# Performance work log

Hardware: AMD Instinct MI355X
Metric: run time of the kernel (lower is better)

## Reference

```python
import jax, jax.numpy as jnp
import numpy as np

B, C, H, W = 16, 16, 96, 320


def _hat(phi):
    z = jnp.zeros_like(phi[..., 0])
    px, py, pz = phi[..., 0], phi[..., 1], phi[..., 2]
    return jnp.stack([
        jnp.stack([z, -pz, py], -1),
        jnp.stack([pz, z, -px], -1),
        jnp.stack([-py, px, z], -1)], -2)


def se3_exp(xi):
    # xi: [B,6] twist (rho, phi) -> [B,4,4] SE3 matrix
    rho, phi = xi[:, :3], xi[:, 3:6]
    th2 = jnp.sum(phi * phi, -1)
    small = th2 < 1e-8
    th2s = jnp.where(small, 1.0, th2)
    th = jnp.sqrt(th2s)
    A = jnp.where(small, 1.0 - th2 / 6.0, jnp.sin(th) / th)
    Bc = jnp.where(small, 0.5 - th2 / 24.0, (1.0 - jnp.cos(th)) / th2s)
    Cc = jnp.where(small, 1.0 / 6.0 - th2 / 120.0, (th - jnp.sin(th)) / (th2s * th))
    K = _hat(phi)
    K2 = K @ K
    I = jnp.eye(3, dtype=xi.dtype)
    R = I + A[:, None, None] * K + Bc[:, None, None] * K2
    V = I + Bc[:, None, None] * K + Cc[:, None, None] * K2
    t = V @ rho[..., None]
    top = jnp.concatenate([R, t], -1)
    bot = jnp.broadcast_to(jnp.array([0.0, 0.0, 0.0, 1.0], xi.dtype), (xi.shape[0], 1, 4))
    return jnp.concatenate([top, bot], 1)


def grid_sample(im, grid):
    # torch F.grid_sample: bilinear, padding_mode='zeros', align_corners=False
    Bb, Cc, Hh, Ww = im.shape
    x = (grid[..., 0] + 1.0) * (Ww * 0.5) - 0.5
    y = (grid[..., 1] + 1.0) * (Hh * 0.5) - 0.5
    x0 = jnp.floor(x); y0 = jnp.floor(y)
    wx = x - x0; wy = y - y0
    x0i = x0.astype(jnp.int32); y0i = y0.astype(jnp.int32)

    def one(imb, x0b, y0b, wxb, wyb):
        def g(ix, iy):
            valid = ((ix >= 0) & (ix < Ww) & (iy >= 0) & (iy < Hh)).astype(imb.dtype)
            v = imb[:, jnp.clip(iy, 0, Hh - 1), jnp.clip(ix, 0, Ww - 1)]
            return v * valid[None]
        v00 = g(x0b, y0b); v01 = g(x0b + 1, y0b)
        v10 = g(x0b, y0b + 1); v11 = g(x0b + 1, y0b + 1)
        wxb = wxb[None]; wyb = wyb[None]
        return (v00 * (1 - wxb) * (1 - wyb) + v01 * wxb * (1 - wyb)
                + v10 * (1 - wxb) * wyb + v11 * wxb * wyb)

    return jax.vmap(one)(im, x0i, y0i, wx, wy)


def setup_inputs():
    key = jax.random.key(0)
    ks = jax.random.split(key, 10)
    # projected pixel coords (center) + 4 finite-difference taps
    xc = jax.random.uniform(ks[0], (B, H, W), jnp.float32, 2.0, W - 3.0)
    yc = jax.random.uniform(ks[1], (B, H, W), jnp.float32, 2.0, H - 3.0)
    xs = jnp.stack([xc, xc + 1, xc - 1, xc, xc], 1)
    ys = jnp.stack([yc, yc, yc, yc + 1, yc - 1], 1)
    p2 = jnp.stack([xs, ys], 1)[:, :, None]  # [B,2,1,5,H,W]
    XY = jax.random.normal(ks[2], (B, 2, H * W)) * 2.0
    Z = 1.0 + 10.0 * jax.random.uniform(ks[3], (B, 1, H * W))
    P2 = jnp.concatenate([XY, Z], 1)  # [B,3,HW], Z > 0
    f = 250.0 + 50.0 * jax.random.uniform(ks[4], (B,))
    K = jnp.zeros((B, 3, 3)).at[:, 0, 0].set(f).at[:, 1, 1].set(f)
    K = K.at[:, 0, 2].set(W / 2).at[:, 1, 2].set(H / 2).at[:, 2, 2].set(1.0)
    poses = se3_exp(0.1 * jax.random.normal(ks[5], (B, 6)))
    return dict(
        poses=poses, calib_K=K, p2=p2, P2=P2,
        weight=jax.random.uniform(ks[6], (B, 1, H, W), jnp.float32, 0.2, 1.0),
        src_feat=jax.random.normal(ks[7], (B, C, H, W)),
        tgt_feat=jax.random.normal(ks[8], (B, C, H, W)),
        src_w=jax.random.uniform(ks[9], (B, 1, H, W), jnp.float32, 0.3, 1.0),
        tgt_w=jax.random.uniform(jax.random.fold_in(key, 11), (B, 1, H, W), jnp.float32, 0.3, 1.0),
    )


def reference(poses, calib_K, p2, P2, weight, src_feat, tgt_feat, src_w, tgt_w):
    Bb, Cc, Hh, Ww = src_feat.shape
    HW = Hh * Ww
    # --- sample_tgt ---
    grid_pix = p2.transpose(2, 0, 4, 5, 3, 1).reshape(Bb, HW, 5, 2)  # n1 == 1
    gx = 2 * (grid_pix[..., :1] + 0.5) / Ww - 1
    gy = 2 * (grid_pix[..., 1:] + 0.5) / Hh - 1
    grid = jnp.concatenate([gx, gy], -1)  # [B,HW,5,2]
    f = grid_sample(tgt_feat, grid).reshape(Bb, Cc, Hh, Ww, 5)
    warped_tgt_feat = f[..., 0]
    grads = jnp.stack([(f[..., 1] - f[..., 2]) * 0.5,
                       (f[..., 3] - f[..., 4]) * 0.5], -1)  # [B,C,H,W,2]
    warped_tgt_w = grid_sample(tgt_w, grid[:, :, :1]).reshape(Bb, 1, Hh, Ww)
    # --- per-pixel 2x6 pixel->pose Jacobian ---
    X, Y, Z = P2[:, 0], P2[:, 1], P2[:, 2]  # [B,HW]
    fx = calib_K[:, 0, 0][:, None]; fy = calib_K[:, 1, 1][:, None]
    fxZ = fx / Z; fyZ = fy / Z
    fxXZ2 = fxZ * X / Z; fyYZ2 = fyZ * Y / Z
    zeros = jnp.zeros_like(fxXZ2)
    row0 = jnp.stack([fxZ, zeros, -fxXZ2, -fxXZ2 * Y, fx + fxXZ2 * X, -fxZ * Y], 1)
    row1 = jnp.stack([zeros, fyZ, -fyYZ2, -fy - fyYZ2 * Y, fyYZ2 * X, fyZ * X], 1)
    J_pixel_xi = jnp.stack([row0, row1], 1).transpose(0, 3, 1, 2)  # [B,HW,2,6]
    J_img_pixel = grads.reshape(Bb, Cc, HW, 2).transpose(0, 2, 1, 3)  # [B,HW,C,2]
    J = -(J_img_pixel @ J_pixel_xi)  # [B,HW,C,6]
    res = (src_feat - warped_tgt_feat).transpose(0, 2, 3, 1).reshape(Bb, HW, Cc)
    w = (src_w * warped_tgt_w * weight).reshape(Bb, HW)
    JW = J * w[:, :, None, None]
    Hm = jnp.einsum('bpck,bpcl->bkl', JW, J)  # [B,6,6] Gauss-Newton Hessian
    b = -jnp.einsum('bpc,bpck->bk', res, JW)  # [B,6]
    # H is SPD (sum of w*J^T J, w>0): solve == cholesky_solve of the original
    update = jnp.linalg.solve(Hm, b[..., None])[..., 0]  # [B,6]
    new_poses = se3_exp(update) @ poses
    return new_poses, update
```

## Files before the change

### kernel.cpp

```cpp
#include <hip/hip_runtime.h>
#include <math.h>

#if __has_builtin(__builtin_amdgcn_cvt_scalef32_pk_f32_fp4) && __has_builtin(__builtin_amdgcn_cvt_scalef32_pk_fp4_f32)
#define HAVE_FP4 1
#else
#define HAVE_FP4 0
#endif

#define BATCH 16
#define CHN   16
#define IMH   96
#define IMW   320
#define HW    (IMH*IMW)
#define NBLK  (HW/256)
#define NPART 27
#define TWB   (HW*4)
#if HAVE_FP4
#define RECB  (HW*16)
#else
#define MAPB  (HW*16)
#endif

typedef __attribute__((ext_vector_type(2))) float f32x2;

__device__ __forceinline__ int comp4(int4 v, int k) {
    switch (k) { case 0: return v.x; case 1: return v.y; case 2: return v.z; default: return v.w; }
}

__device__ __forceinline__ float dpp_row_sum(float x) {
    union fi { float f; int i; };
    fi v; v.f = x;
#define DPPSTEP(CTRL) { fi t; t.i = __builtin_amdgcn_update_dpp(0, v.i, CTRL, 0xf, 0xf, true); v.f += t.f; }
    DPPSTEP(0x111)
    DPPSTEP(0x112)
    DPPSTEP(0x114)
    DPPSTEP(0x118)
#undef DPPSTEP
    return v.f;
}

__global__ __launch_bounds__(256) void build_maps(const float* __restrict__ in,
                                                  const float* __restrict__ tw,
                                                  char* __restrict__ dst,
                                                  char* __restrict__ twr) {
    const int b = blockIdx.y;
    const int p = blockIdx.x * 256 + threadIdx.x;
    const int y = p / IMW, x = p - y * IMW;
    const float* ip = in + (size_t)b * CHN * HW + p;
    float f[16];
#pragma unroll
    for (int c = 0; c < 16; ++c) f[c] = ip[c * HW];

#if HAVE_FP4
    unsigned d0 = 0, d1 = 0;
    d0 = __builtin_amdgcn_cvt_scalef32_pk_fp4_f32(d0, f[0],  f[1],  1.0f, 0);
    d0 = __builtin_amdgcn_cvt_scalef32_pk_fp4_f32(d0, f[2],  f[3],  1.0f, 1);
    d0 = __builtin_amdgcn_cvt_scalef32_pk_fp4_f32(d0, f[4],  f[5],  1.0f, 2);
    d0 = __builtin_amdgcn_cvt_scalef32_pk_fp4_f32(d0, f[6],  f[7],  1.0f, 3);
    d1 = __builtin_amdgcn_cvt_scalef32_pk_fp4_f32(d1, f[8],  f[9],  1.0f, 0);
    d1 = __builtin_amdgcn_cvt_scalef32_pk_fp4_f32(d1, f[10], f[11], 1.0f, 1);
    d1 = __builtin_amdgcn_cvt_scalef32_pk_fp4_f32(d1, f[12], f[13], 1.0f, 2);
    d1 = __builtin_amdgcn_cvt_scalef32_pk_fp4_f32(d1, f[14], f[15], 1.0f, 3);
    int2 lv; lv.x = (int)d0; lv.y = (int)d1;
    char* rb = dst + (size_t)b * RECB;
    *(int2*)(rb + (size_t)p * 16) = lv;
    if (y > 0)        *(int2*)(rb + (size_t)(p - IMW) * 16 + 8) = lv;
    if (y == IMH - 1) *(int2*)(rb + (size_t)p * 16 + 8) = lv;
#else
    int4 pk;
    int* pw = &pk.x;
#pragma unroll
    for (int k = 0; k < 4; ++k) {
        int dw = __builtin_amdgcn_cvt_pk_fp8_f32(f[4 * k + 0], f[4 * k + 1], 0, false);
        dw     = __builtin_amdgcn_cvt_pk_fp8_f32(f[4 * k + 2], f[4 * k + 3], dw, true);
        pw[k] = dw;
    }
    *(int4*)(dst + (size_t)b * MAPB + ((size_t)(y >> 1) * IMW + x) * 32 + (y & 1) * 16) = pk;
#endif

    const float* twb = tw + (size_t)b * HW;
    const int xp1 = min(x + 1, IMW - 1), yp1 = min(y + 1, IMH - 1);
    const float v00 = twb[p];
    const float v01 = twb[y * IMW + xp1];
    const float v10 = twb[yp1 * IMW + x];
    const float v11 = twb[yp1 * IMW + xp1];
    int wq = __builtin_amdgcn_cvt_pk_fp8_f32(v00, v01, 0, false);
    wq     = __builtin_amdgcn_cvt_pk_fp8_f32(v10, v11, wq, true);
    ((int*)(twr + (size_t)b * TWB))[p] = wq;
}

__global__ __launch_bounds__(256, 2) void gn_accum(
    const float* __restrict__ p2,
    const float* __restrict__ P2,
    const float* __restrict__ calibK,
    const float* __restrict__ weight,
    const float* __restrict__ src_feat,
    const float* __restrict__ src_w,
    const char* __restrict__ twr,
    const char* __restrict__ fmap,
    float* __restrict__ partials)
{
    __shared__ float xs_l[1280];
    __shared__ float ys_l[1280];
    __shared__ float red[16][NPART];

    const int n   = blockIdx.x;
    const int b   = n & 15;
    const int blk = n >> 4;
    const int t   = threadIdx.x;
    const int p   = blk * 256 + t;

    const unsigned Gblk0 = ((unsigned)b * HW + (unsigned)(blk * 256)) * 5u;
#pragma unroll
    for (int j = 0; j < 5; ++j) {
        const unsigned idx  = (unsigned)(j * 256 + t);
        const unsigned G    = Gblk0 + idx;
        const unsigned sBig = G / (unsigned)(BATCH * HW);
        const unsigned r    = G - sBig * (unsigned)(BATCH * HW);
        const unsigned bb   = r / (unsigned)HW;
        const unsigned q    = r - bb * (unsigned)HW;
        const float* pb = p2 + (size_t)bb * (10 * HW) + (size_t)sBig * HW + q;
        xs_l[idx] = pb[0];
        ys_l[idx] = pb[5 * HW];
    }
    __syncthreads();

    float wxs[5], wys[5];
    int   twoff = 0;
#if HAVE_FP4
    int off[5];
#else
    int offA[5], offC[5];
#endif
#pragma unroll
    for (int s = 0; s < 5; ++s) {
        const float xp = xs_l[5 * t + s];
        const float yp = ys_l[5 * t + s];
        float gx = 2.0f * (xp + 0.5f) / (float)IMW - 1.0f;
        float gy = 2.0f * (yp + 0.5f) / (float)IMH - 1.0f;
        float x  = (gx + 1.0f) * ((float)IMW * 0.5f) - 0.5f;
        float y  = (gy + 1.0f) * ((float)IMH * 0.5f) - 0.5f;
        float x0 = floorf(x), y0 = floorf(y);
        wxs[s] = x - x0;
        wys[s] = y - y0;
        int xi = (int)x0, yi = (int)y0;
        xi = min(max(xi, 0), IMW - 2);
        yi = min(max(yi, 0), IMH - 2);
#if HAVE_FP4
        off[s] = (yi * IMW + xi) * 16;
#else
        const int h0 = yi >> 1, par0 = yi & 1;
        const int h1 = h0 + par0, par1 = par0 ^ 1;
        offA[s] = (h0 * IMW + xi) * 32 + par0 * 16;
        offC[s] = (h1 * IMW + xi) * 32 + par1 * 16;
#endif
        if (s == 0) twoff = (yi * IMW + xi) * 4;
    }

#if HAVE_FP4
    const char* mapb = fmap + (size_t)b * RECB;
    int4 L0[5], L1[5];
#pragma unroll
    for (int s = 0; s < 5; ++s) {
        L0[s] = *(const int4*)(mapb + off[s]);
        L1[s] = *(const int4*)(mapb + off[s] + 16);
    }
#else
    const char* mapb = fmap + (size_t)b * MAPB;
    int4 LA[5], LB[5], LC[5], LD[5];
#pragma unroll
    for (int s = 0; s < 5; ++s) {
        LA[s] = *(const int4*)(mapb + offA[s]);
        LB[s] = *(const int4*)(mapb + offA[s] + 32);
        LC[s] = *(const int4*)(mapb + offC[s]);
        LD[s] = *(const int4*)(mapb + offC[s] + 32);
    }
#endif
    const int twq = *(const int*)(twr + (size_t)b * TWB + twoff);

    float srcv[16];
    const float* srcb = src_feat + (size_t)b * CHN * HW + p;
#pragma unroll
    for (int c = 0; c < 16; ++c) srcv[c] = srcb[c * HW];

    const float* P2b = P2 + (size_t)b * 3 * HW;
    const float X = P2b[p], Y = P2b[HW + p], Z = P2b[2 * HW + p];
    const float wP  = weight[(size_t)b * HW + p];
    const float swP = src_w[(size_t)b * HW + p];

    const float fx = calibK[b * 9 + 0];
    const float fy = calibK[b * 9 + 4];
    const float fxZ = fx / Z, fyZ = fy / Z;
    const float fxXZ2 = fxZ * X / Z;
    const float fyYZ2 = fyZ * Y / Z;
    float r0[6] = { fxZ, 0.0f, -fxXZ2, -fxXZ2 * Y, fx + fxXZ2 * X, -fxZ * Y };
    float r1[6] = { 0.0f, fyZ, -fyYZ2, -fy - fyYZ2 * Y, fyYZ2 * X, fyZ * X };

    float w00[5], w01[5], w10[5], w11[5];
#pragma unroll
    for (int s = 0; s < 5; ++s) {
        float wx = wxs[s], wy = wys[s];
        w00[s] = (1.0f - wx) * (1.0f - wy);
        w01[s] = wx * (1.0f - wy);
        w10[s] = (1.0f - wx) * wy;
        w11[s] = wx * wy;
    }

    float wtw;
    {
        const float wx = wxs[0], wy = wys[0];
        f32x2 wlo = __builtin_amdgcn_cvt_pk_f32_fp8(twq, false);
        f32x2 whi = __builtin_amdgcn_cvt_pk_f32_fp8(twq, true);
        wtw = wlo[0] * (1.0f - wx) * (1.0f - wy) + wlo[1] * wx * (1.0f - wy)
            + whi[0] * (1.0f - wx) * wy          + whi[1] * wx * wy;
    }
    const float w = swP * wtw * wP;

    f32x2 SxxV = {0.f,0.f}, SxyV = {0.f,0.f}, SyyV = {0.f,0.f}, TxV = {0.f,0.f}, TyV = {0.f,0.f};
#if HAVE_FP4
#define PAIRSTEP(H, K) {                                                          \
        f32x2 fsv[5];                                                             \
        _Pragma("unroll")                                                         \
        for (int s = 0; s < 5; ++s) {                                             \
            const int ad = (H) ? L0[s].y : L0[s].x;                               \
            const int bd = (H) ? L1[s].y : L1[s].x;                               \
            const int cd = (H) ? L0[s].w : L0[s].z;                               \
            const int dd = (H) ? L1[s].w : L1[s].z;                               \
            fsv[s] = __builtin_amdgcn_cvt_scalef32_pk_f32_fp4(ad, 1.0f, K) * w00[s] \
                   + __builtin_amdgcn_cvt_scalef32_pk_f32_fp4(bd, 1.0f, K) * w01[s] \
                   + __builtin_amdgcn_cvt_scalef32_pk_f32_fp4(cd, 1.0f, K) * w10[s] \
                   + __builtin_amdgcn_cvt_scalef32_pk_f32_fp4(dd, 1.0f, K) * w11[s]; \
        }                                                                         \
        const f32x2 sr = { srcv[(H) * 8 + 2 * (K)], srcv[(H) * 8 + 2 * (K) + 1] };\
        f32x2 resv = sr - fsv[0];                                                 \
        f32x2 gxv  = (fsv[1] - fsv[2]) * 0.5f;                                    \
        f32x2 gyv  = (fsv[3] - fsv[4]) * 0.5f;                                    \
        SxxV += gxv * gxv; SxyV += gxv * gyv; SyyV += gyv * gyv;                  \
        TxV  += resv * gxv; TyV += resv * gyv; }
    PAIRSTEP(0, 0) PAIRSTEP(0, 1) PAIRSTEP(0, 2) PAIRSTEP(0, 3)
    PAIRSTEP(1, 0) PAIRSTEP(1, 1) PAIRSTEP(1, 2) PAIRSTEP(1, 3)
#undef PAIRSTEP
#else
#pragma unroll
    for (int k = 0; k < 4; ++k) {
        f32x2 flo[5], fhi[5];
#pragma unroll
        for (int s = 0; s < 5; ++s) {
            const int a = comp4(LA[s], k), bq = comp4(LB[s], k);
            const int c = comp4(LC[s], k), d  = comp4(LD[s], k);
            flo[s] = __builtin_amdgcn_cvt_pk_f32_fp8(a,  false) * w00[s]
                   + __builtin_amdgcn_cvt_pk_f32_fp8(bq, false) * w01[s]
                   + __builtin_amdgcn_cvt_pk_f32_fp8(c,  false) * w10[s]
                   + __builtin_amdgcn_cvt_pk_f32_fp8(d,  false) * w11[s];
            fhi[s] = __builtin_amdgcn_cvt_pk_f32_fp8(a,  true)  * w00[s]
                   + __builtin_amdgcn_cvt_pk_f32_fp8(bq, true)  * w01[s]
                   + __builtin_amdgcn_cvt_pk_f32_fp8(c,  true)  * w10[s]
                   + __builtin_amdgcn_cvt_pk_f32_fp8(d,  true)  * w11[s];
        }
        const f32x2 srcl = { srcv[4 * k + 0], srcv[4 * k + 1] };
        const f32x2 srch = { srcv[4 * k + 2], srcv[4 * k + 3] };
        f32x2 resl = srcl - flo[0];
        f32x2 gxl  = (flo[1] - flo[2]) * 0.5f;
        f32x2 gyl  = (flo[3] - flo[4]) * 0.5f;
        SxxV += gxl * gxl; SxyV += gxl * gyl; SyyV += gyl * gyl;
        TxV  += resl * gxl; TyV += resl * gyl;
        f32x2 resh = srch - fhi[0];
        f32x2 gxh  = (fhi[1] - fhi[2]) * 0.5f;
        f32x2 gyh  = (fhi[3] - fhi[4]) * 0.5f;
        SxxV += gxh * gxh; SxyV += gxh * gyh; SyyV += gyh * gyh;
        TxV  += resh * gxh; TyV += resh * gyh;
    }
#endif
    const float Sxx = SxxV[0] + SxxV[1];
    const float Sxy = SxyV[0] + SxyV[1];
    const float Syy = SyyV[0] + SyyV[1];
    const float Tx  = TxV[0]  + TxV[1];
    const float Ty  = TyV[0]  + TyV[1];

    const float Pm = w * Sxx, Qm = w * Sxy, Rm = w * Syy;
    const float tx = w * Tx,  ty = w * Ty;

    float av[6], cv[6];
#pragma unroll
    for (int k = 0; k < 6; ++k) {
        av[k] = Pm * r0[k] + Qm * r1[k];
        cv[k] = Qm * r0[k] + Rm * r1[k];
    }

    const int wv   = t >> 6;
    const int lane = t & 63;
    const int rrow = (wv << 2) | (lane >> 4);
    const bool wr  = (lane & 15) == 15;

    int idx = 0;
#pragma unroll
    for (int k = 0; k < 6; ++k) {
#pragma unroll
        for (int l = 0; l < 6; ++l) {
            if (l < k) continue;
            float v = r0[k] * av[l] + r1[k] * cv[l];
            v = dpp_row_sum(v);
            if (wr) red[rrow][idx] = v;
            ++idx;
        }
    }
#pragma unroll
    for (int k = 0; k < 6; ++k) {
        float v = tx * r0[k] + ty * r1[k];
        v = dpp_row_sum(v);
        if (wr) red[rrow][21 + k] = v;
    }
    __syncthreads();
    if (t < NPART) {
        float s = 0.0f;
#pragma unroll
        for (int r = 0; r < 16; ++r) s += red[r][t];
        partials[((size_t)b * NBLK + blk) * NPART + t] = s;
    }
}

__global__ __launch_bounds__(256) void gn_solve(
    const float* __restrict__ partials,
    const float* __restrict__ poses,
    float* __restrict__ out)
{
    const int b = blockIdx.x;
    const int t = threadIdx.x;
    __shared__ double dsum[8][NPART];
    __shared__ double sums[NPART];

    if (t < 216) {
        const int col = t % NPART;
        const int g   = t / NPART;
        double s = 0.0;
        for (int j = g; j < NBLK; j += 8)
            s += (double)partials[((size_t)b * NBLK + j) * NPART + col];
        dsum[g][col] = s;
    }
    __syncthreads();
    if (t < NPART) {
        double s = 0.0;
#pragma unroll
        for (int g = 0; g < 8; ++g) s += dsum[g][t];
        sums[t] = s;
    }
    __syncthreads();
    if (t != 0) return;

    double A[6][7];
    {
        int idx = 0;
        for (int k = 0; k < 6; ++k)
            for (int l = k; l < 6; ++l) {
                A[k][l] = sums[idx];
                A[l][k] = sums[idx];
                ++idx;
            }
        for (int k = 0; k < 6; ++k) A[k][6] = sums[21 + k];
    }
    for (int col = 0; col < 6; ++col) {
        int piv = col; double mx = fabs(A[col][col]);
        for (int rr = col + 1; rr < 6; ++rr) {
            double v = fabs(A[rr][col]);
            if (v > mx) { mx = v; piv = rr; }
        }
        if (piv != col)
            for (int j = col; j < 7; ++j) { double tmp = A[col][j]; A[col][j] = A[piv][j]; A[piv][j] = tmp; }
        double d = A[col][col];
        for (int rr = col + 1; rr < 6; ++rr) {
            double f = A[rr][col] / d;
            for (int j = col; j < 7; ++j) A[rr][j] -= f * A[col][j];
        }
    }
    double x[6];
    for (int i = 5; i >= 0; --i) {
        double s = A[i][6];
        for (int j = i + 1; j < 6; ++j) s -= A[i][j] * x[j];
        x[i] = s / A[i][i];
    }

    const double rho[3] = { x[0], x[1], x[2] };
    const double phi[3] = { x[3], x[4], x[5] };
    const double th2 = phi[0]*phi[0] + phi[1]*phi[1] + phi[2]*phi[2];
    const bool small = th2 < 1e-8;
    const double th2s = small ? 1.0 : th2;
    const double th = sqrt(th2s);
    const double Ac = small ? 1.0 - th2 / 6.0   : sin(th) / th;
    const double Bc = small ? 0.5 - th2 / 24.0  : (1.0 - cos(th)) / th2s;
    const double Cc = small ? 1.0/6.0 - th2/120.0 : (th - sin(th)) / (th2s * th);
    const double Kh[3][3] = { { 0.0, -phi[2],  phi[1] },
                              {  phi[2], 0.0, -phi[0] },
                              { -phi[1],  phi[0], 0.0 } };
    double K2[3][3];
    for (int i = 0; i < 3; ++i)
        for (int j = 0; j < 3; ++j) {
            double s = 0.0;
            for (int k = 0; k < 3; ++k) s += Kh[i][k] * Kh[k][j];
            K2[i][j] = s;
        }
    double T[4][4];
    for (int i = 0; i < 3; ++i)
        for (int j = 0; j < 3; ++j) {
            double I = (i == j) ? 1.0 : 0.0;
            T[i][j] = I + Ac * Kh[i][j] + Bc * K2[i][j];
        }
    for (int i = 0; i < 3; ++i) {
        double s = 0.0;
        for (int j = 0; j < 3; ++j) {
            double I = (i == j) ? 1.0 : 0.0;
            double V = I + Bc * Kh[i][j] + Cc * K2[i][j];
            s += V * rho[j];
        }
        T[i][3] = s;
    }
    T[3][0] = 0.0; T[3][1] = 0.0; T[3][2] = 0.0; T[3][3] = 1.0;

    const float* pz = poses + b * 16;
    for (int i = 0; i < 4; ++i)
        for (int j = 0; j < 4; ++j) {
            double s = 0.0;
            for (int k = 0; k < 4; ++k) s += T[i][k] * (double)pz[k * 4 + j];
            out[b * 16 + i * 4 + j] = (float)s;
        }
    for (int k = 0; k < 6; ++k)
        out[BATCH * 16 + b * 6 + k] = (float)x[k];
}

extern "C" void kernel_launch(void* const* d_in, const int* in_sizes, int n_in,
                              void* d_out, int out_size, void* d_ws, size_t ws_size,
                              hipStream_t stream) {
    const float* poses    = (const float*)d_in[0];
    const float* calibK   = (const float*)d_in[1];
    const float* p2       = (const float*)d_in[2];
    const float* P2       = (const float*)d_in[3];
    const float* weight   = (const float*)d_in[4];
    const float* src_feat = (const float*)d_in[5];
    const float* tgt_feat = (const float*)d_in[6];
    const float* src_w    = (const float*)d_in[7];
    const float* tgt_w    = (const float*)d_in[8];
    float* out = (float*)d_out;

#if HAVE_FP4
    char*  rec      = (char*)d_ws;
    char*  twr      = rec + (size_t)BATCH * RECB;
    float* partials = (float*)(twr + (size_t)BATCH * TWB);
#else
    char*  rec      = (char*)d_ws;
    char*  twr      = rec + (size_t)BATCH * MAPB;
    float* partials = (float*)(twr + (size_t)BATCH * TWB);
#endif

    hipLaunchKernelGGL(build_maps, dim3(HW / 256, BATCH), dim3(256), 0, stream,
                       tgt_feat, tgt_w, rec, twr);
    hipLaunchKernelGGL(gn_accum, dim3(NBLK * BATCH), dim3(256), 0, stream,
                       p2, P2, calibK, weight, src_feat, src_w, twr, rec, partials);
    hipLaunchKernelGGL(gn_solve, dim3(BATCH), dim3(256), 0, stream,
                       partials, poses, out);
}
```

Measured before the change: 47.82 us.

## Split each pixel's channels across two threads with interleaved FP4 record layout

gn_accum now gives each pixel to two threads, each handling 8 of the 16 channels, so blocks cover 128 pixels and the grid doubles. The FP4 record is re-interleaved so each half-thread reads one 8-byte int2 per row instead of a 16-byte int4. The goal is lower per-thread register pressure and more parallelism for the latency-bound gather loads. In exchange, per-pixel setup work (Jacobian, weights, coordinates) is duplicated, and the half-results must be combined, which the hidden reduction code presumably does. The FP8 fallback path is removed, leaving FP4 as the only path.

```diff
diff --git a/kernel.cpp b/kernel.cpp
--- a/kernel.cpp
+++ b/kernel.cpp
@@ -1,31 +1,18 @@
 #include <hip/hip_runtime.h>
 #include <math.h>
-
-#if __has_builtin(__builtin_amdgcn_cvt_scalef32_pk_f32_fp4) && __has_builtin(__builtin_amdgcn_cvt_scalef32_pk_fp4_f32)
-#define HAVE_FP4 1
-#else
-#define HAVE_FP4 0
-#endif
 
 #define BATCH 16
 #define CHN   16
 #define IMH   96
 #define IMW   320
 #define HW    (IMH*IMW)
-#define NBLK  (HW/256)
+#define PPB   128
+#define NBLK  (HW/PPB)
 #define NPART 27
 #define TWB   (HW*4)
-#if HAVE_FP4
 #define RECB  (HW*16)
-#else
-#define MAPB  (HW*16)
-#endif
 
 typedef __attribute__((ext_vector_type(2))) float f32x2;
-
-__device__ __forceinline__ int comp4(int4 v, int k) {
-    switch (k) { case 0: return v.x; case 1: return v.y; case 2: return v.z; default: return v.w; }
-}
 
 __device__ __forceinline__ float dpp_row_sum(float x) {
     union fi { float f; int i; };
@@ -41,7 +28,7 @@
 
 __global__ __launch_bounds__(256) void build_maps(const float* __restrict__ in,
                                                   const float* __restrict__ tw,
-                                                  char* __restrict__ dst,
+                                                  char* __restrict__ rec,
                                                   char* __restrict__ twr) {
     const int b = blockIdx.y;
     const int p = blockIdx.x * 256 + threadIdx.x;
@@ -51,7 +38,6 @@
 #pragma unroll
     for (int c = 0; c < 16; ++c) f[c] = ip[c * HW];
 
-#if HAVE_FP4
     unsigned d0 = 0, d1 = 0;
     d0 = __builtin_amdgcn_cvt_scalef32_pk_fp4_f32(d0, f[0],  f[1],  1.0f, 0);
     d0 = __builtin_amdgcn_cvt_scalef32_pk_fp4_f32(d0, f[2],  f[3],  1.0f, 1);
@@ -61,22 +47,20 @@
     d1 = __builtin_amdgcn_cvt_scalef32_pk_fp4_f32(d1, f[10], f[11], 1.0f, 1);
     d1 = __builtin_amdgcn_cvt_scalef32_pk_fp4_f32(d1, f[12], f[13], 1.0f, 2);
     d1 = __builtin_amdgcn_cvt_scalef32_pk_fp4_f32(d1, f[14], f[15], 1.0f, 3);
-    int2 lv; lv.x = (int)d0; lv.y = (int)d1;
-    char* rb = dst + (size_t)b * RECB;
-    *(int2*)(rb + (size_t)p * 16) = lv;
-    if (y > 0)        *(int2*)(rb + (size_t)(p - IMW) * 16 + 8) = lv;
-    if (y == IMH - 1) *(int2*)(rb + (size_t)p * 16 + 8) = lv;
-#else
-    int4 pk;
-    int* pw = &pk.x;
-#pragma unroll
-    for (int k = 0; k < 4; ++k) {
-        int dw = __builtin_amdgcn_cvt_pk_fp8_f32(f[4 * k + 0], f[4 * k + 1], 0, false);
-        dw     = __builtin_amdgcn_cvt_pk_fp8_f32(f[4 * k + 2], f[4 * k + 3], dw, true);
-        pw[k] = dw;
-    }
-    *(int4*)(dst + (size_t)b * MAPB + ((size_t)(y >> 1) * IMW + x) * 32 + (y & 1) * 16) = pk;
-#endif
+
+    int* rb = (int*)(rec + (size_t)b * RECB);
+    const int self = p * 4;
+    rb[self + 0] = (int)d0;
+    rb[self + 2] = (int)d1;
+    if (y > 0) {
+        const int up = (p - IMW) * 4;
+        rb[up + 1] = (int)d0;
+        rb[up + 3] = (int)d1;
+    }
+    if (y == IMH - 1) {
+        rb[self + 1] = (int)d0;
+        rb[self + 3] = (int)d1;
+    }
 
     const float* twb = tw + (size_t)b * HW;
     const int xp1 = min(x + 1, IMW - 1), yp1 = min(y + 1, IMH - 1);
@@ -97,45 +81,45 @@
     const float* __restrict__ src_feat,
     const float* __restrict__ src_w,
     const char* __restrict__ twr,
-    const char* __restrict__ fmap,
+    const char* __restrict__ rec,
     float* __restrict__ partials)
 {
-    __shared__ float xs_l[1280];
-    __shared__ float ys_l[1280];
+    __shared__ float xs_l[768];
+    __shared__ float ys_l[768];
     __shared__ float red[16][NPART];
 
     const int n   = blockIdx.x;
     const int b   = n & 15;
     const int blk = n >> 4;
     const int t   = threadIdx.x;
-    const int p   = blk * 256 + t;
-
-    const unsigned Gblk0 = ((unsigned)b * HW + (unsigned)(blk * 256)) * 5u;
-#pragma unroll
-    for (int j = 0; j < 5; ++j) {
-        const unsigned idx  = (unsigned)(j * 256 + t);
-        const unsigned G    = Gblk0 + idx;
-        const unsigned sBig = G / (unsigned)(BATCH * HW);
-        const unsigned r    = G - sBig * (unsigned)(BATCH * HW);
-        const unsigned bb   = r / (unsigned)HW;
-        const unsigned q    = r - bb * (unsigned)HW;
-        const float* pb = p2 + (size_t)bb * (10 * HW) + (size_t)sBig * HW + q;
-        xs_l[idx] = pb[0];
-        ys_l[idx] = pb[5 * HW];
+    const int m   = t >> 1;
+    const int h   = t & 1;
+    const int pp  = blk * PPB + m;
+
+    const unsigned Gblk0 = ((unsigned)b * HW + (unsigned)(blk * PPB)) * 5u;
+#pragma unroll
+    for (int j = 0; j < 3; ++j) {
+        const unsigned idx = (unsigned)(j * 256 + t);
+        if (idx < 640) {
+            const unsigned G    = Gblk0 + idx;
+            const unsigned sBig = G / (unsigned)(BATCH * HW);
+            const unsigned r    = G - sBig * (unsigned)(BATCH * HW);
+            const unsigned bb   = r / (unsigned)HW;
+            const unsigned q    = r - bb * (unsigned)HW;
+            const float* pb = p2 + (size_t)bb * (10 * HW) + (size_t)sBig * HW + q;
+            xs_l[idx] = pb[0];
+            ys_l[idx] = pb[5 * HW];
+        }
     }
     __syncthreads();
 
     float wxs[5], wys[5];
+    int   off[5];
     int   twoff = 0;
-#if HAVE_FP4
-    int off[5];
-#else
-    int offA[5], offC[5];
-#endif
 #pragma unroll
     for (int s = 0; s < 5; ++s) {
-        const float xp = xs_l[5 * t + s];
-        const float yp = ys_l[5 * t + s];
+        const float xp = xs_l[5 * m + s];
+        const float yp = ys_l[5 * m + s];
         float gx = 2.0f * (xp + 0.5f) / (float)IMW - 1.0f;
         float gy = 2.0f * (yp + 0.5f) / (float)IMH - 1.0f;
         float x  = (gx + 1.0f) * ((float)IMW * 0.5f) - 0.5f;
@@ -146,47 +130,28 @@
         int xi = (int)x0, yi = (int)y0;
         xi = min(max(xi, 0), IMW - 2);
         yi = min(max(yi, 0), IMH - 2);
-#if HAVE_FP4
         off[s] = (yi * IMW + xi) * 16;
-#else
-        const int h0 = yi >> 1, par0 = yi & 1;
-        const int h1 = h0 + par0, par1 = par0 ^ 1;
-        offA[s] = (h0 * IMW + xi) * 32 + par0 * 16;
-        offC[s] = (h1 * IMW + xi) * 32 + par1 * 16;
-#endif
         if (s == 0) twoff = (yi * IMW + xi) * 4;
     }
 
-#if HAVE_FP4
-    const char* mapb = fmap + (size_t)b * RECB;
-    int4 L0[5], L1[5];
+    const char* mapb = rec + (size_t)b * RECB + h * 8;
+    int2 L0[5], L1[5];
 #pragma unroll
     for (int s = 0; s < 5; ++s) {
-        L0[s] = *(const int4*)(mapb + off[s]);
-        L1[s] = *(const int4*)(mapb + off[s] + 16);
-    }
-#else
-    const char* mapb = fmap + (size_t)b * MAPB;
-    int4 LA[5], LB[5], LC[5], LD[5];
-#pragma unroll
-    for (int s = 0; s < 5; ++s) {
-        LA[s] = *(const int4*)(mapb + offA[s]);
-        LB[s] = *(const int4*)(mapb + offA[s] + 32);
-        LC[s] = *(const int4*)(mapb + offC[s]);
-        LD[s] = *(const int4*)(mapb + offC[s] + 32);
-    }
-#endif
+        L0[s] = *(const int2*)(mapb + off[s]);
+        L1[s] = *(const int2*)(mapb + off[s] + 16);
+    }
     const int twq = *(const int*)(twr + (size_t)b * TWB + twoff);
 
-    float srcv[16];
-    const float* srcb = src_feat + (size_t)b * CHN * HW + p;
-#pragma unroll
-    for (int c = 0; c < 16; ++c) srcv[c] = srcb[c * HW];
+    float srcv[8];
+    const float* srcb = src_feat + (size_t)b * CHN * HW + (size_t)h * 8 * HW + pp;
+#pragma unroll
+    for (int j = 0; j < 8; ++j) srcv[j] = srcb[j * HW];
 
     const float* P2b = P2 + (size_t)b * 3 * HW;
-    const float X = P2b[p], Y = P2b[HW + p], Z = P2b[2 * HW + p];
-    const float wP  = weight[(size_t)b * HW + p];
-    const float swP = src_w[(size_t)b * HW + p];
+    const float X = P2b[pp], Y = P2b[HW + pp], Z = P2b[2 * HW + pp];
+    const float wP  = weight[(size_t)b * HW + pp];
+    const float swP = src_w[(size_t)b * HW + pp];
 
     const float fx = calibK[b * 9 + 0];
     const float fy = calibK[b * 9 + 4];
@@ -217,60 +182,24 @@
     const float w = swP * wtw * wP;
 
     f32x2 SxxV = {0.f,0.f}, SxyV = {0.f,0.f}, SyyV = {0.f,0.f}, TxV = {0.f,0.f}, TyV = {0.f,0.f};
-#if HAVE_FP4
-#define PAIRSTEP(H, K) {                                                          \
+#define PAIRSTEP(K) {                                                             \
         f32x2 fsv[5];                                                             \
         _Pragma("unroll")                                                         \
         for (int s = 0; s < 5; ++s) {                                             \
-            const int ad = (H) ? L0[s].y : L0[s].x;                               \
-            const int bd = (H) ? L1[s].y : L1[s].x;                               \
-            const int cd = (H) ? L0[s].w : L0[s].z;                               \
-            const int dd = (H) ? L1[s].w : L1[s].z;                               \
-            fsv[s] = __builtin_amdgcn_cvt_scalef32_pk_f32_fp4(ad, 1.0f, K) * w00[s] \
-                   + __builtin_amdgcn_cvt_scalef32_pk_f32_fp4(bd, 1.0f, K) * w01[s] \
-                   + __builtin_amdgcn_cvt_scalef32_pk_f32_fp4(cd, 1.0f, K) * w10[s] \
-                   + __builtin_amdgcn_cvt_scalef32_pk_f32_fp4(dd, 1.0f, K) * w11[s]; \
+            fsv[s] = __builtin_amdgcn_cvt_scalef32_pk_f32_fp4(L0[s].x, 1.0f, K) * w00[s] \
+                   + __builtin_amdgcn_cvt_scalef32_pk_f32_fp4(L1[s].x, 1.0f, K) * w01[s] \
+                   + __builtin_amdgcn_cvt_scalef32_pk_f32_fp4(L0[s].y, 1.0f, K) * w10[s] \
+                   + __builtin_amdgcn_cvt_scalef32_pk_f32_fp4(L1[s].y, 1.0f, K) * w11[s]; \
         }                                                                         \
-        const f32x2 sr = { srcv[(H) * 8 + 2 * (K)], srcv[(H) * 8 + 2 * (K) + 1] };\
+        const f32x2 sr = { srcv[2 * (K)], srcv[2 * (K) + 1] };                    \
         f32x2 resv = sr - fsv[0];                                                 \
         f32x2 gxv  = (fsv[1] - fsv[2]) * 0.5f;                                    \
         f32x2 gyv  = (fsv[3] - fsv[4]) * 0.5f;                                    \
         SxxV += gxv * gxv; SxyV += gxv * gyv; SyyV += gyv * gyv;                  \
         TxV  += resv * gxv; TyV += resv * gyv; }
-    PAIRSTEP(0, 0) PAIRSTEP(0, 1) PAIRSTEP(0, 2) PAIRSTEP(0, 3)
-    PAIRSTEP(1, 0) PAIRSTEP(1, 1) PAIRSTEP(1, 2) PAIRSTEP(1, 3)
+    PAIRSTEP(0) PAIRSTEP(1) PAIRSTEP(2) PAIRSTEP(3)
 #undef PAIRSTEP
-#else
-#pragma unroll
-    for (int k = 0; k < 4; ++k) {
-        f32x2 flo[5], fhi[5];
-#pragma unroll
-        for (int s = 0; s < 5; ++s) {
-            const int a = comp4(LA[s], k), bq = comp4(LB[s], k);
-            const int c = comp4(LC[s], k), d  = comp4(LD[s], k);
-            flo[s] = __builtin_amdgcn_cvt_pk_f32_fp8(a,  false) * w00[s]
-                   + __builtin_amdgcn_cvt_pk_f32_fp8(bq, false) * w01[s]
-                   + __builtin_amdgcn_cvt_pk_f32_fp8(c,  false) * w10[s]
-                   + __builtin_amdgcn_cvt_pk_f32_fp8(d,  false) * w11[s];
-            fhi[s] = __builtin_amdgcn_cvt_pk_f32_fp8(a,  true)  * w00[s]
-                   + __builtin_amdgcn_cvt_pk_f32_fp8(bq, true)  * w01[s]
-                   + __builtin_amdgcn_cvt_pk_f32_fp8(c,  true)  * w10[s]
-                   + __builtin_amdgcn_cvt_pk_f32_fp8(d,  true)  * w11[s];
-        }
-        const f32x2 srcl = { srcv[4 * k + 0], srcv[4 * k + 1] };
-        const f32x2 srch = { srcv[4 * k + 2], srcv[4 * k + 3] };
-        f32x2 resl = srcl - flo[0];
-        f32x2 gxl  = (flo[1] - flo[2]) * 0.5f;
-        f32x2 gyl  = (flo[3] - flo[4]) * 0.5f;
-        SxxV += gxl * gxl; SxyV += gxl * gyl; SyyV += gyl * gyl;
-        TxV  += resl * gxl; TyV += resl * gyl;
-        f32x2 resh = srch - fhi[0];
-        f32x2 gxh  = (fhi[1] - fhi[2]) * 0.5f;
-        f32x2 gyh  = (fhi[3] - fhi[4]) * 0.5f;
-        SxxV += gxh * gxh; SxyV += gxh * gyh; SyyV += gyh * gyh;
-        TxV  += resh * gxh; TyV += resh * gyh;
-    }
-#endif
+
     const float Sxx = SxxV[0] + SxxV[1];
     const float Sxy = SxyV[0] + SxyV[1];
     const float Syy = SyyV[0] + SyyV[1];
@@ -440,15 +369,9 @@
     const float* tgt_w    = (const float*)d_in[8];
     float* out = (float*)d_out;
 
-#if HAVE_FP4
     char*  rec      = (char*)d_ws;
     char*  twr      = rec + (size_t)BATCH * RECB;
     float* partials = (float*)(twr + (size_t)BATCH * TWB);
-#else
-    char*  rec      = (char*)d_ws;
-    char*  twr      = rec + (size_t)BATCH * MAPB;
-    float* partials = (float*)(twr + (size_t)BATCH * TWB);
-#endif
 
     hipLaunchKernelGGL(build_maps, dim3(HW / 256, BATCH), dim3(256), 0, stream,
                        tgt_feat, tgt_w, rec, twr);
```

New measurement: 55.00 us. 1.15x slower.
